# Optimization experiments

Measured on AMD Instinct MI355X. Metric: run time of the kernel, lower is better.

Reference implementation:

```python
import jax, jax.numpy as jnp
import numpy as np

N = 64        # SSM state size
L = 4096      # sequence / kernel length (l_max)
BH = 4096     # batch * channels


def setup_inputs() -> dict:
    key = jax.random.key(0)
    ks = jax.random.split(key, 8)
    u = jax.random.normal(ks[0], (BH, L), dtype=jnp.float32)
    # S4D-Lin style eigenvalue init: Re = -0.5, Im = pi * n
    Lambda_re = -0.5 * jnp.ones((N,), dtype=jnp.float32)
    Lambda_im = jnp.pi * jnp.arange(N, dtype=jnp.float32)
    P_re = jax.random.normal(ks[1], (N,), dtype=jnp.float32) * (0.5 ** 0.5)
    P_im = jax.random.normal(ks[2], (N,), dtype=jnp.float32) * (0.5 ** 0.5)
    B_re = jax.random.normal(ks[3], (N,), dtype=jnp.float32)
    B_im = jax.random.normal(ks[4], (N,), dtype=jnp.float32)
    C_ri = jax.random.normal(ks[5], (N, 2), dtype=jnp.float32) * (0.5 ** 0.5)
    D = jnp.ones((1,), dtype=jnp.float32)
    # log_step ~ uniform(log(0.001), log(0.1)) as in log_step_initializer
    log_step = jax.random.uniform(ks[6], (1,), dtype=jnp.float32,
                                  minval=jnp.log(0.001), maxval=jnp.log(0.1))
    return {"u": u, "Lambda_re": Lambda_re, "Lambda_im": Lambda_im,
            "P_re": P_re, "P_im": P_im, "B_re": B_re, "B_im": B_im,
            "C_ri": C_ri, "D": D, "log_step": log_step}


def kernel_DPLR(Lambda, P, Q, B, C, step, length):
    # Evaluate the SSM generating function at the roots of unity via 4 Cauchy dots,
    # then inverse FFT to recover the length-L convolution kernel.
    Omega_L = jnp.exp((-2j * jnp.pi) * (jnp.arange(length) / length))  # (L,)
    a0, a1 = jnp.conj(C), jnp.conj(Q)
    b0, b1 = B, P
    g = (2.0 / step) * ((1.0 - Omega_L) / (1.0 + Omega_L))  # (L,)
    c = 2.0 / (1.0 + Omega_L)                               # (L,)

    def cauchy(v):  # v: (N,) -> (L,)
        return (v[None, :] / (g[:, None] - Lambda[None, :])).sum(-1)

    k00 = cauchy(a0 * b0)
    k01 = cauchy(a0 * b1)
    k10 = cauchy(a1 * b0)
    k11 = cauchy(a1 * b1)
    at_roots = c * (k00 - k01 * (1.0 / (1.0 + k11)) * k10)
    return jnp.fft.ifft(at_roots, length).real  # (L,)


def causal_convolution(u, K):
    # FFT-based linear (causal) convolution; u: (..., L), K: (L,)
    n = 2 * u.shape[-1]
    ud = jnp.fft.rfft(u, n=n, axis=-1)
    Kd = jnp.fft.rfft(K, n=n)
    return jnp.fft.irfft(ud * Kd, n=n, axis=-1)[..., : u.shape[-1]]


def reference(u, Lambda_re, Lambda_im, P_re, P_im, B_re, B_im, C_ri, D, log_step):
    Lambda = Lambda_re + 1j * Lambda_im
    P = P_re + 1j * P_im
    B = B_re + 1j * B_im
    C = C_ri[..., 0] + 1j * C_ri[..., 1]
    step = jnp.exp(log_step)  # (1,)
    K = kernel_DPLR(Lambda, P, P, B, C, step, u.shape[-1])  # (L,) real
    y_s = causal_convolution(u, K) + D * u  # (BH, L)
    return y_s
```

## Files before the change

### kernel.cpp

```cpp
#include <hip/hip_runtime.h>
#include <math.h>

#define LSEQ 4096
#define MFFT 8192
#define NM   64
#define NBH  4096
#define TMAIN 512

__device__ __forceinline__ float2 cmulf(float2 a, float2 b) {
  return make_float2(a.x*b.x - a.y*b.y, a.x*b.y + a.y*b.x);
}
__device__ __forceinline__ float2 caddf(float2 a, float2 b){ return make_float2(a.x+b.x, a.y+b.y); }
__device__ __forceinline__ float2 csubf(float2 a, float2 b){ return make_float2(a.x-b.x, a.y-b.y); }
__device__ __forceinline__ float2 conjf(float2 a){ return make_float2(a.x, -a.y); }

__device__ __forceinline__ void r4_fwd(float2& x0, float2& x1, float2& x2, float2& x3,
                                       float2 w1, float2 w2, float2 w3) {
  float2 A = caddf(x0,x2), C = csubf(x0,x2);
  float2 B = caddf(x1,x3), D = csubf(x1,x3);
  float2 y1 = make_float2(C.x + D.y, C.y - D.x);
  float2 y3 = make_float2(C.x - D.y, C.y + D.x);
  x0 = caddf(A,B);
  x1 = cmulf(y1,w1);
  x2 = cmulf(csubf(A,B),w2);
  x3 = cmulf(y3,w3);
}
__device__ __forceinline__ void r4_inv(float2& y0, float2& y1, float2& y2, float2& y3,
                                       float2 w1c, float2 w2c, float2 w3c) {
  float2 c1 = cmulf(y1,w1c);
  float2 c2 = cmulf(y2,w2c);
  float2 c3 = cmulf(y3,w3c);
  float2 ap = caddf(y0,c2), bp = csubf(y0,c2);
  float2 cp = caddf(c1,c3);
  float2 dp = make_float2(c3.y - c1.y, c1.x - c3.x);
  y0 = caddf(ap,cp); y1 = caddf(bp,dp); y2 = csubf(ap,cp); y3 = csubf(bp,dp);
}

#define DECL_CONSTS \
  const float C16R[4]={1.f,0.9238795325112867f,0.7071067811865476f,0.3826834323650898f}; \
  const float C16I[4]={0.f,-0.3826834323650898f,-0.7071067811865476f,-0.9238795325112867f}; \
  const float C8R[4] ={1.f,0.7071067811865476f,0.f,-0.7071067811865476f}; \
  const float C8I[4] ={0.f,-0.7071067811865476f,-1.f,-0.7071067811865476f}; \
  const float C163R[4]={1.f,0.3826834323650898f,-0.7071067811865476f,-0.9238795325112867f}; \
  const float C163I[4]={0.f,-0.9238795325112867f,-0.7071067811865476f,0.3826834323650898f};

__device__ __forceinline__ void r16_fwd(float2 x[16], float2 wA) {
  DECL_CONSTS
  float2 wA2 = cmulf(wA,wA), wA3 = cmulf(wA2,wA);
  #pragma unroll
  for (int k0 = 0; k0 < 4; k0++) {
    float2 w1 = cmulf(wA,  make_float2(C16R[k0],C16I[k0]));
    float2 w2 = cmulf(wA2, make_float2(C8R[k0], C8I[k0]));
    float2 w3 = cmulf(wA3, make_float2(C163R[k0],C163I[k0]));
    r4_fwd(x[k0], x[k0+4], x[k0+8], x[k0+12], w1, w2, w3);
  }
  float2 wB = cmulf(wA2,wA2);
  float2 wB2 = cmulf(wB,wB), wB3 = cmulf(wB2,wB);
  #pragma unroll
  for (int q = 0; q < 4; q++)
    r4_fwd(x[4*q], x[4*q+1], x[4*q+2], x[4*q+3], wB, wB2, wB3);
}
__device__ __forceinline__ void r16_inv(float2 x[16], float2 wA) {
  DECL_CONSTS
  float2 wA2 = cmulf(wA,wA), wA3 = cmulf(wA2,wA);
  float2 wB = cmulf(wA2,wA2);
  float2 wB2 = cmulf(wB,wB), wB3 = cmulf(wB2,wB);
  float2 wBc = conjf(wB), wB2c = conjf(wB2), wB3c = conjf(wB3);
  #pragma unroll
  for (int q = 0; q < 4; q++)
    r4_inv(x[4*q], x[4*q+1], x[4*q+2], x[4*q+3], wBc, wB2c, wB3c);
  #pragma unroll
  for (int k0 = 0; k0 < 4; k0++) {
    float2 w1c = conjf(cmulf(wA,  make_float2(C16R[k0],C16I[k0])));
    float2 w2c = conjf(cmulf(wA2, make_float2(C8R[k0], C8I[k0])));
    float2 w3c = conjf(cmulf(wA3, make_float2(C163R[k0],C163I[k0])));
    r4_inv(x[k0], x[k0+4], x[k0+8], x[k0+12], w1c, w2c, w3c);
  }
}

__global__ void tables_kernel(float2* __restrict__ ctg) {
  int t = blockIdx.x*blockDim.x + threadIdx.x;
  if (t >= 560) return;
  int e = (t < 512) ? t : (t < 544) ? 16*(t-512) : 256*(t-544);
  double ang = -2.0*M_PI*(double)e/(double)MFFT;
  ctg[t] = make_float2((float)cos(ang), (float)sin(ang));
}

__global__ void cauchy_kernel(const float* __restrict__ Lre, const float* __restrict__ Lim,
                              const float* __restrict__ Pre, const float* __restrict__ Pim,
                              const float* __restrict__ Bre, const float* __restrict__ Bim,
                              const float* __restrict__ Cri, const float* __restrict__ lstep,
                              float2* __restrict__ a_out) {
  int k = blockIdx.x*blockDim.x + threadIdx.x;
  if (k >= LSEQ) return;
  double step = exp((double)lstep[0]);
  double ang = -2.0*M_PI*(double)k/(double)LSEQ;
  double wr = cos(ang), wi = sin(ang);
  double nr = 1.0 - wr, ni = -wi;
  double dr = 1.0 + wr, di = wi;
  double dn = dr*dr + di*di;
  double gre = (2.0/step) * (nr*dr + ni*di)/dn;
  double gim = (2.0/step) * (ni*dr - nr*di)/dn;
  double cre = 2.0*dr/dn, cim = -2.0*di/dn;
  double k00r=0,k00i=0,k01r=0,k01i=0,k10r=0,k10i=0,k11r=0,k11i=0;
  for (int n = 0; n < NM; n++) {
    double lre = Lre[n], lim = Lim[n];
    double pre = Pre[n], pim = Pim[n];
    double bre = Bre[n], bim = Bim[n];
    double ccr = Cri[2*n], cci = Cri[2*n+1];
    double er = gre - lre, ei = gim - lim;
    double inv = 1.0/(er*er + ei*ei);
    double ir =  er*inv, ii = -ei*inv;
    double v00r = ccr*bre + cci*bim, v00i = ccr*bim - cci*bre;
    double v01r = ccr*pre + cci*pim, v01i = ccr*pim - cci*pre;
    double v10r = pre*bre + pim*bim, v10i = pre*bim - pim*bre;
    double v11r = pre*pre + pim*pim, v11i = 0.0;
    k00r += v00r*ir - v00i*ii;  k00i += v00r*ii + v00i*ir;
    k01r += v01r*ir - v01i*ii;  k01i += v01r*ii + v01i*ir;
    k10r += v10r*ir - v10i*ii;  k10i += v10r*ii + v10i*ir;
    k11r += v11r*ir - v11i*ii;  k11i += v11r*ii + v11i*ir;
  }
  double numr = k01r*k10r - k01i*k10i, numi = k01r*k10i + k01i*k10r;
  double der = 1.0 + k11r, dei = k11i;
  double dinv = 1.0/(der*der + dei*dei);
  double qr = (numr*der + numi*dei)*dinv;
  double qi = (numi*der - numr*dei)*dinv;
  double tr = k00r - qr, ti = k00i - qi;
  double ar = cre*tr - cim*ti, ai = cre*ti + cim*tr;
  a_out[k] = make_float2((float)ar, (float)ai);
}

__global__ void ktime_kernel(const float2* __restrict__ a, float* __restrict__ K) {
  int lane = threadIdx.x & 63;
  int l = blockIdx.x * (blockDim.x >> 6) + (threadIdx.x >> 6);
  if (l >= LSEQ) return;
  double ang0 = 2.0*M_PI*(double)((l*lane) & (LSEQ-1))/(double)LSEQ;
  double tr = cos(ang0), ti = sin(ang0);
  double ang1 = 2.0*M_PI*(double)(l & 63)/64.0;
  double wr = cos(ang1), wi = sin(ang1);
  double acc = 0.0;
  for (int k = 0; k < 64; k++) {
    float2 ak = a[lane + (k << 6)];
    acc += (double)ak.x*tr - (double)ak.y*ti;
    double ntr = tr*wr - ti*wi;
    ti = tr*wi + ti*wr;
    tr = ntr;
  }
  for (int off = 32; off > 0; off >>= 1) acc += __shfl_down(acc, off);
  if (lane == 0) K[l] = (float)(acc/(double)LSEQ);
}

__global__ void kd_kernel(const float* __restrict__ K, const float2* __restrict__ ctg,
                          float2* __restrict__ Kd) {
  __shared__ float2 z[MFFT];
  const int tid = threadIdx.x;
  float2 x[16];
  #pragma unroll
  for (int k = 0; k < 8; k++) x[k] = make_float2(K[tid + 512*k], 0.f);
  #pragma unroll
  for (int k = 8; k < 16; k++) x[k] = make_float2(0.f, 0.f);
  r16_fwd(x, ctg[tid]);
  {
    int xc = (tid >> 5) & 15; int p0 = tid ^ xc;
    #pragma unroll
    for (int k = 0; k < 16; k++) z[p0 + 512*k] = x[k];
  }
  __syncthreads();
  const int j5 = tid & 31;
  const int Gb = (tid >> 5) << 9;
  #pragma unroll
  for (int k = 0; k < 16; k++) x[k] = z[Gb + 32*k + (j5 ^ k)];
  r16_fwd(x, ctg[512 + j5]);
  {
    bool hi = (tid >> 4) & 1;
    float2 w32 = ctg[544 + (tid & 15)];
    float2 weff = hi ? w32 : make_float2(1.f, 0.f);
    float s = hi ? -1.f : 1.f;
    #pragma unroll
    for (int k = 0; k < 16; k++) {
      float rx = __shfl_xor(x[k].x, 16);
      float ry = __shfl_xor(x[k].y, 16);
      float2 pre = make_float2(fmaf(x[k].x, s, rx), fmaf(x[k].y, s, ry));
      x[k] = cmulf(pre, weff);
    }
  }
  #pragma unroll
  for (int k = 0; k < 16; k++) z[Gb + 32*k + (j5 ^ k)] = x[k];
  __syncthreads();
  {
    int xc = (tid >> 1) & 15; int b16 = tid << 4;
    #pragma unroll
    for (int c = 0; c < 16; c++) x[c] = z[b16 + (c ^ xc)];
    r16_fwd(x, make_float2(1.f, 0.f));
    const float sc = 1.0f/(float)MFFT;
    #pragma unroll
    for (int c = 0; c < 16; c++)
      Kd[b16 + c] = make_float2(x[c].x*sc, x[c].y*sc);
  }
}

__global__ __launch_bounds__(TMAIN, 2)
void conv_kernel(const float* __restrict__ u, const float* __restrict__ Dp,
                 const float2* __restrict__ ctg, const float2* __restrict__ Kd,
                 float* __restrict__ out) {
  __shared__ float2 z[MFFT];
  const int tid = threadIdx.x;
  const int r0 = blockIdx.x, r1 = blockIdx.x + (NBH/2);
  const float* u0 = u + (size_t)r0*LSEQ;
  const float* u1 = u + (size_t)r1*LSEQ;
  float2 x[16];
  #pragma unroll
  for (int k = 0; k < 8; k++)
    x[k] = make_float2(u0[tid + 512*k], u1[tid + 512*k]);
  #pragma unroll
  for (int k = 8; k < 16; k++) x[k] = make_float2(0.f, 0.f);
  const float2 wA1 = ctg[tid];
  r16_fwd(x, wA1);
  {
    int xc = (tid >> 5) & 15; int p0 = tid ^ xc;
    #pragma unroll
    for (int k = 0; k < 16; k++) z[p0 + 512*k] = x[k];
  }
  __syncthreads();
  const int j5 = tid & 31;
  const int Gb = (tid >> 5) << 9;
  #pragma unroll
  for (int k = 0; k < 16; k++) x[k] = z[Gb + 32*k + (j5 ^ k)];
  const float2 wA2t = ctg[512 + j5];
  r16_fwd(x, wA2t);
  {
    bool hi = (tid >> 4) & 1;
    float2 w32 = ctg[544 + (tid & 15)];
    float2 weff = hi ? w32 : make_float2(1.f, 0.f);
    float s = hi ? -1.f : 1.f;
    #pragma unroll
    for (int k = 0; k < 16; k++) {
      float rx = __shfl_xor(x[k].x, 16);
      float ry = __shfl_xor(x[k].y, 16);
      float2 pre = make_float2(fmaf(x[k].x, s, rx), fmaf(x[k].y, s, ry));
      x[k] = cmulf(pre, weff);
    }
  }
  #pragma unroll
  for (int k = 0; k < 16; k++) z[Gb + 32*k + (j5 ^ k)] = x[k];
  __syncthreads();
  {
    int xc = (tid >> 1) & 15; int b16 = tid << 4;
    #pragma unroll
    for (int c = 0; c < 16; c++) x[c] = z[b16 + (c ^ xc)];
    float4 kd[8];
    const float4* Kd4 = (const float4*)(Kd + b16);
    #pragma unroll
    for (int q = 0; q < 8; q++) kd[q] = Kd4[q];
    r16_fwd(x, make_float2(1.f, 0.f));
    #pragma unroll
    for (int c = 0; c < 8; c++) {
      x[2*c]   = cmulf(x[2*c],   make_float2(kd[c].x, kd[c].y));
      x[2*c+1] = cmulf(x[2*c+1], make_float2(kd[c].z, kd[c].w));
    }
    r16_inv(x, make_float2(1.f, 0.f));
    #pragma unroll
    for (int c = 0; c < 16; c++) z[b16 + (c ^ xc)] = x[c];
  }
  __syncthreads();
  {
    #pragma unroll
    for (int k = 0; k < 16; k++) x[k] = z[Gb + 32*k + (j5 ^ k)];
    bool hi = (tid >> 4) & 1;
    float2 w32 = ctg[544 + (tid & 15)];
    float2 weffc = hi ? conjf(w32) : make_float2(1.f, 0.f);
    float s = hi ? -1.f : 1.f;
    #pragma unroll
    for (int k = 0; k < 16; k++) {
      float2 v = cmulf(x[k], weffc);
      float rx = __shfl_xor(v.x, 16);
      float ry = __shfl_xor(v.y, 16);
      x[k] = make_float2(fmaf(v.x, s, rx), fmaf(v.y, s, ry));
    }
    r16_inv(x, wA2t);
    #pragma unroll
    for (int k = 0; k < 16; k++) z[Gb + 32*k + (j5 ^ k)] = x[k];
  }
  __syncthreads();
  {
    int xc = (tid >> 5) & 15; int p0 = tid ^ xc;
    #pragma unroll
    for (int k = 0; k < 16; k++) x[k] = z[p0 + 512*k];
    r16_inv(x, wA1);
    const float Dv = Dp[0];
    float* o0 = out + (size_t)r0*LSEQ;
    float* o1 = out + (size_t)r1*LSEQ;
    #pragma unroll
    for (int k = 0; k < 8; k++) {
      int idx = tid + 512*k;
      o0[idx] = x[k].x + Dv*u0[idx];
      o1[idx] = x[k].y + Dv*u1[idx];
    }
  }
}

extern "C" void kernel_launch(void* const* d_in, const int* in_sizes, int n_in,
                              void* d_out, int out_size, void* d_ws, size_t ws_size,
                              hipStream_t stream) {
  const float* u     = (const float*)d_in[0];
  const float* Lre   = (const float*)d_in[1];
  const float* Lim   = (const float*)d_in[2];
  const float* Pre   = (const float*)d_in[3];
  const float* Pim   = (const float*)d_in[4];
  const float* Bre   = (const float*)d_in[5];
  const float* Bim   = (const float*)d_in[6];
  const float* Cri   = (const float*)d_in[7];
  const float* Dp    = (const float*)d_in[8];
  const float* lstep = (const float*)d_in[9];
  float* out = (float*)d_out;

  char* ws = (char*)d_ws;
  float2* a_ws  = (float2*)(ws);
  float*  K_ws  = (float*)(ws + 32768);
  float2* Kd_ws = (float2*)(ws + 49152);
  float2* ct_ws = (float2*)(ws + 114688);

  hipLaunchKernelGGL(tables_kernel, dim3(3),    dim3(256), 0, stream, ct_ws);
  hipLaunchKernelGGL(cauchy_kernel, dim3(64),   dim3(64),  0, stream,
                     Lre, Lim, Pre, Pim, Bre, Bim, Cri, lstep, a_ws);
  hipLaunchKernelGGL(ktime_kernel,  dim3(1024), dim3(256), 0, stream, a_ws, K_ws);
  hipLaunchKernelGGL(kd_kernel,     dim3(1),    dim3(TMAIN), 0, stream,
                     K_ws, ct_ws, Kd_ws);
  hipLaunchKernelGGL(conv_kernel,   dim3(NBH/2), dim3(TMAIN), 0, stream,
                     u, Dp, ct_ws, Kd_ws, out);
}
```

Measured before the change: 126.2 us.

## Fold D skip into kernel spectrum, precompute twiddle tables, use wave barriers

```diff
diff --git a/kernel.cpp b/kernel.cpp
--- a/kernel.cpp
+++ b/kernel.cpp
@@ -9,6 +9,9 @@
 
 __device__ __forceinline__ float2 cmulf(float2 a, float2 b) {
   return make_float2(a.x*b.x - a.y*b.y, a.x*b.y + a.y*b.x);
+}
+__device__ __forceinline__ float2 cmulc(float2 a, float2 b) {
+  return make_float2(a.x*b.x + a.y*b.y, a.y*b.x - a.x*b.y);
 }
 __device__ __forceinline__ float2 caddf(float2 a, float2 b){ return make_float2(a.x+b.x, a.y+b.y); }
 __device__ __forceinline__ float2 csubf(float2 a, float2 b){ return make_float2(a.x-b.x, a.y-b.y); }
@@ -35,6 +38,16 @@
   float2 dp = make_float2(c3.y - c1.y, c1.x - c3.x);
   y0 = caddf(ap,cp); y1 = caddf(bp,dp); y2 = csubf(ap,cp); y3 = csubf(bp,dp);
 }
+__device__ __forceinline__ void r4_invc(float2& y0, float2& y1, float2& y2, float2& y3,
+                                        float2 w1, float2 w2, float2 w3) {
+  float2 c1 = cmulc(y1,w1);
+  float2 c2 = cmulc(y2,w2);
+  float2 c3 = cmulc(y3,w3);
+  float2 ap = caddf(y0,c2), bp = csubf(y0,c2);
+  float2 cp = caddf(c1,c3);
+  float2 dp = make_float2(c3.y - c1.y, c1.x - c3.x);
+  y0 = caddf(ap,cp); y1 = caddf(bp,dp); y2 = csubf(ap,cp); y3 = csubf(bp,dp);
+}
 
 #define DECL_CONSTS \
   const float C16R[4]={1.f,0.9238795325112867f,0.7071067811865476f,0.3826834323650898f}; \
@@ -44,46 +57,97 @@
   const float C163R[4]={1.f,0.3826834323650898f,-0.7071067811865476f,-0.9238795325112867f}; \
   const float C163I[4]={0.f,-0.9238795325112867f,-0.7071067811865476f,0.3826834323650898f};
 
-__device__ __forceinline__ void r16_fwd(float2 x[16], float2 wA) {
+__device__ __forceinline__ void r16_fwd1(float2 x[16]) {
   DECL_CONSTS
-  float2 wA2 = cmulf(wA,wA), wA3 = cmulf(wA2,wA);
-  #pragma unroll
-  for (int k0 = 0; k0 < 4; k0++) {
-    float2 w1 = cmulf(wA,  make_float2(C16R[k0],C16I[k0]));
-    float2 w2 = cmulf(wA2, make_float2(C8R[k0], C8I[k0]));
-    float2 w3 = cmulf(wA3, make_float2(C163R[k0],C163I[k0]));
-    r4_fwd(x[k0], x[k0+4], x[k0+8], x[k0+12], w1, w2, w3);
-  }
-  float2 wB = cmulf(wA2,wA2);
-  float2 wB2 = cmulf(wB,wB), wB3 = cmulf(wB2,wB);
+  #pragma unroll
+  for (int k0 = 0; k0 < 4; k0++)
+    r4_fwd(x[k0], x[k0+4], x[k0+8], x[k0+12],
+           make_float2(C16R[k0],C16I[k0]), make_float2(C8R[k0],C8I[k0]),
+           make_float2(C163R[k0],C163I[k0]));
   #pragma unroll
   for (int q = 0; q < 4; q++)
-    r4_fwd(x[4*q], x[4*q+1], x[4*q+2], x[4*q+3], wB, wB2, wB3);
-}
-__device__ __forceinline__ void r16_inv(float2 x[16], float2 wA) {
+    r4_fwd(x[4*q], x[4*q+1], x[4*q+2], x[4*q+3],
+           make_float2(1.f,0.f), make_float2(1.f,0.f), make_float2(1.f,0.f));
+}
+__device__ __forceinline__ void r16_inv1(float2 x[16]) {
   DECL_CONSTS
-  float2 wA2 = cmulf(wA,wA), wA3 = cmulf(wA2,wA);
-  float2 wB = cmulf(wA2,wA2);
-  float2 wB2 = cmulf(wB,wB), wB3 = cmulf(wB2,wB);
-  float2 wBc = conjf(wB), wB2c = conjf(wB2), wB3c = conjf(wB3);
   #pragma unroll
   for (int q = 0; q < 4; q++)
-    r4_inv(x[4*q], x[4*q+1], x[4*q+2], x[4*q+3], wBc, wB2c, wB3c);
-  #pragma unroll
-  for (int k0 = 0; k0 < 4; k0++) {
-    float2 w1c = conjf(cmulf(wA,  make_float2(C16R[k0],C16I[k0])));
-    float2 w2c = conjf(cmulf(wA2, make_float2(C8R[k0], C8I[k0])));
-    float2 w3c = conjf(cmulf(wA3, make_float2(C163R[k0],C163I[k0])));
-    r4_inv(x[k0], x[k0+4], x[k0+8], x[k0+12], w1c, w2c, w3c);
-  }
-}
-
-__global__ void tables_kernel(float2* __restrict__ ctg) {
+    r4_invc(x[4*q], x[4*q+1], x[4*q+2], x[4*q+3],
+            make_float2(1.f,0.f), make_float2(1.f,0.f), make_float2(1.f,0.f));
+  #pragma unroll
+  for (int k0 = 0; k0 < 4; k0++)
+    r4_invc(x[k0], x[k0+4], x[k0+8], x[k0+12],
+            make_float2(C16R[k0],C16I[k0]), make_float2(C8R[k0],C8I[k0]),
+            make_float2(C163R[k0],C163I[k0]));
+}
+
+__device__ __forceinline__ void r16_fwd_t(float2 x[16], const float4 tp[8]) {
+  float2 tw[16];
+  #pragma unroll
+  for (int q = 0; q < 8; q++) {
+    tw[2*q]   = make_float2(tp[q].x, tp[q].y);
+    tw[2*q+1] = make_float2(tp[q].z, tp[q].w);
+  }
+  #pragma unroll
+  for (int k0 = 0; k0 < 4; k0++)
+    r4_fwd(x[k0], x[k0+4], x[k0+8], x[k0+12], tw[k0], tw[4+k0], tw[8+k0]);
+  #pragma unroll
+  for (int q = 0; q < 4; q++)
+    r4_fwd(x[4*q], x[4*q+1], x[4*q+2], x[4*q+3], tw[12], tw[13], tw[14]);
+}
+__device__ __forceinline__ void r16_inv_t(float2 x[16], const float4 tp[8]) {
+  float2 tw[16];
+  #pragma unroll
+  for (int q = 0; q < 8; q++) {
+    tw[2*q]   = make_float2(tp[q].x, tp[q].y);
+    tw[2*q+1] = make_float2(tp[q].z, tp[q].w);
+  }
+  #pragma unroll
+  for (int q = 0; q < 4; q++)
+    r4_invc(x[4*q], x[4*q+1], x[4*q+2], x[4*q+3], tw[12], tw[13], tw[14]);
+  #pragma unroll
+  for (int k0 = 0; k0 < 4; k0++)
+    r4_invc(x[k0], x[k0+4], x[k0+8], x[k0+12], tw[k0], tw[4+k0], tw[8+k0]);
+}
+
+__device__ __forceinline__ float2 Wexp(long long e) {
+  double ang = -2.0*M_PI*(double)(e & (MFFT-1))/(double)MFFT;
+  return make_float2((float)cos(ang), (float)sin(ang));
+}
+__global__ void tables_kernel(float4* __restrict__ tp1, float4* __restrict__ tp2,
+                              float2* __restrict__ ct2) {
   int t = blockIdx.x*blockDim.x + threadIdx.x;
-  if (t >= 560) return;
-  int e = (t < 512) ? t : (t < 544) ? 16*(t-512) : 256*(t-544);
-  double ang = -2.0*M_PI*(double)e/(double)MFFT;
-  ctg[t] = make_float2((float)cos(ang), (float)sin(ang));
+  if (t < 512) {
+    float2 w[16];
+    #pragma unroll
+    for (int i = 0; i < 4; i++) {
+      w[i]   = Wexp((long long)t   + 512LL*i);
+      w[4+i] = Wexp(2LL*t + 1024LL*i);
+      w[8+i] = Wexp(3LL*t + 1536LL*i);
+    }
+    w[12] = Wexp(4LL*t); w[13] = Wexp(8LL*t); w[14] = Wexp(12LL*t);
+    w[15] = make_float2(1.f, 0.f);
+    #pragma unroll
+    for (int q = 0; q < 8; q++)
+      tp1[q*512 + t] = make_float4(w[2*q].x, w[2*q].y, w[2*q+1].x, w[2*q+1].y);
+  } else if (t < 544) {
+    int j = t - 512;
+    float2 w[16];
+    #pragma unroll
+    for (int i = 0; i < 4; i++) {
+      w[i]   = Wexp(16LL*j + 512LL*i);
+      w[4+i] = Wexp(32LL*j + 1024LL*i);
+      w[8+i] = Wexp(48LL*j + 1536LL*i);
+    }
+    w[12] = Wexp(64LL*j); w[13] = Wexp(128LL*j); w[14] = Wexp(192LL*j);
+    w[15] = make_float2(1.f, 0.f);
+    #pragma unroll
+    for (int q = 0; q < 8; q++)
+      tp2[q*32 + j] = make_float4(w[2*q].x, w[2*q].y, w[2*q+1].x, w[2*q+1].y);
+  } else if (t < 560) {
+    ct2[t - 544] = Wexp(256LL*(t - 544));
+  }
 }
 
 __global__ void cauchy_kernel(const float* __restrict__ Lre, const float* __restrict__ Lim,
@@ -150,16 +214,24 @@
   if (lane == 0) K[l] = (float)(acc/(double)LSEQ);
 }
 
-__global__ void kd_kernel(const float* __restrict__ K, const float2* __restrict__ ctg,
-                          float2* __restrict__ Kd) {
+__global__ void kd_kernel(const float* __restrict__ K, const float* __restrict__ Dp,
+                          const float4* __restrict__ tp1, const float4* __restrict__ tp2,
+                          const float2* __restrict__ ct2, float2* __restrict__ Kd) {
   __shared__ float2 z[MFFT];
   const int tid = threadIdx.x;
   float2 x[16];
-  #pragma unroll
-  for (int k = 0; k < 8; k++) x[k] = make_float2(K[tid + 512*k], 0.f);
+  float4 tpr[8];
+  #pragma unroll
+  for (int q = 0; q < 8; q++) tpr[q] = tp1[(q<<9) + tid];
+  #pragma unroll
+  for (int k = 0; k < 8; k++) {
+    float v = K[tid + 512*k];
+    if (tid == 0 && k == 0) v += Dp[0];
+    x[k] = make_float2(v, 0.f);
+  }
   #pragma unroll
   for (int k = 8; k < 16; k++) x[k] = make_float2(0.f, 0.f);
-  r16_fwd(x, ctg[tid]);
+  r16_fwd_t(x, tpr);
   {
     int xc = (tid >> 5) & 15; int p0 = tid ^ xc;
     #pragma unroll
@@ -168,12 +240,15 @@
   __syncthreads();
   const int j5 = tid & 31;
   const int Gb = (tid >> 5) << 9;
+  float4 tq[8];
+  #pragma unroll
+  for (int q = 0; q < 8; q++) tq[q] = tp2[(q<<5) + j5];
   #pragma unroll
   for (int k = 0; k < 16; k++) x[k] = z[Gb + 32*k + (j5 ^ k)];
-  r16_fwd(x, ctg[512 + j5]);
+  r16_fwd_t(x, tq);
   {
     bool hi = (tid >> 4) & 1;
-    float2 w32 = ctg[544 + (tid & 15)];
+    float2 w32 = ct2[tid & 15];
     float2 weff = hi ? w32 : make_float2(1.f, 0.f);
     float s = hi ? -1.f : 1.f;
     #pragma unroll
@@ -191,7 +266,7 @@
     int xc = (tid >> 1) & 15; int b16 = tid << 4;
     #pragma unroll
     for (int c = 0; c < 16; c++) x[c] = z[b16 + (c ^ xc)];
-    r16_fwd(x, make_float2(1.f, 0.f));
+    r16_fwd1(x);
     const float sc = 1.0f/(float)MFFT;
     #pragma unroll
     for (int c = 0; c < 16; c++)
@@ -200,8 +275,9 @@
 }
 
 __global__ __launch_bounds__(TMAIN, 2)
-void conv_kernel(const float* __restrict__ u, const float* __restrict__ Dp,
-                 const float2* __restrict__ ctg, const float2* __restrict__ Kd,
+void conv_kernel(const float* __restrict__ u,
+                 const float4* __restrict__ tp1, const float4* __restrict__ tp2,
+                 const float2* __restrict__ ct2, const float2* __restrict__ Kd,
                  float* __restrict__ out) {
   __shared__ float2 z[MFFT];
   const int tid = threadIdx.x;
@@ -209,14 +285,16 @@
   const float* u0 = u + (size_t)r0*LSEQ;
   const float* u1 = u + (size_t)r1*LSEQ;
   float2 x[16];
-  #pragma unroll
-  for (int k = 0; k < 8; k++)
-    x[k] = make_float2(u0[tid + 512*k], u1[tid + 512*k]);
-  #pragma unroll
-  for (int k = 8; k < 16; k++) x[k] = make_float2(0.f, 0.f);
-  const float2 wA1 = ctg[tid];
-  r16_fwd(x, wA1);
-  {
+  {
+    float4 tpr[8];
+    #pragma unroll
+    for (int q = 0; q < 8; q++) tpr[q] = tp1[(q<<9) + tid];
+    #pragma unroll
+    for (int k = 0; k < 8; k++)
+      x[k] = make_float2(u0[tid + 512*k], u1[tid + 512*k]);
+    #pragma unroll
+    for (int k = 8; k < 16; k++) x[k] = make_float2(0.f, 0.f);
+    r16_fwd_t(x, tpr);
     int xc = (tid >> 5) & 15; int p0 = tid ^ xc;
     #pragma unroll
     for (int k = 0; k < 16; k++) z[p0 + 512*k] = x[k];
@@ -224,26 +302,28 @@
   __syncthreads();
   const int j5 = tid & 31;
   const int Gb = (tid >> 5) << 9;
-  #pragma unroll
-  for (int k = 0; k < 16; k++) x[k] = z[Gb + 32*k + (j5 ^ k)];
-  const float2 wA2t = ctg[512 + j5];
-  r16_fwd(x, wA2t);
-  {
-    bool hi = (tid >> 4) & 1;
-    float2 w32 = ctg[544 + (tid & 15)];
+  const bool hi = (tid >> 4) & 1;
+  const float2 w32 = ct2[tid & 15];
+  const float sgn = hi ? -1.f : 1.f;
+  {
+    float4 tq[8];
+    #pragma unroll
+    for (int q = 0; q < 8; q++) tq[q] = tp2[(q<<5) + j5];
+    #pragma unroll
+    for (int k = 0; k < 16; k++) x[k] = z[Gb + 32*k + (j5 ^ k)];
+    r16_fwd_t(x, tq);
     float2 weff = hi ? w32 : make_float2(1.f, 0.f);
-    float s = hi ? -1.f : 1.f;
     #pragma unroll
     for (int k = 0; k < 16; k++) {
       float rx = __shfl_xor(x[k].x, 16);
       float ry = __shfl_xor(x[k].y, 16);
-      float2 pre = make_float2(fmaf(x[k].x, s, rx), fmaf(x[k].y, s, ry));
+      float2 pre = make_float2(fmaf(x[k].x, sgn, rx), fmaf(x[k].y, sgn, ry));
       x[k] = cmulf(pre, weff);
     }
-  }
-  #pragma unroll
-  for (int k = 0; k < 16; k++) z[Gb + 32*k + (j5 ^ k)] = x[k];
-  __syncthreads();
+    #pragma unroll
+    for (int k = 0; k < 16; k++) z[Gb + 32*k + (j5 ^ k)] = x[k];
+  }
+  __builtin_amdgcn_wave_barrier();
   {
     int xc = (tid >> 1) & 15; int b16 = tid << 4;
     #pragma unroll
@@ -252,49 +332,51 @@
     const float4* Kd4 = (const float4*)(Kd + b16);
     #pragma unroll
     for (int q = 0; q < 8; q++) kd[q] = Kd4[q];
-    r16_fwd(x, make_float2(1.f, 0.f));
+    r16_fwd1(x);
     #pragma unroll
     for (int c = 0; c < 8; c++) {
       x[2*c]   = cmulf(x[2*c],   make_float2(kd[c].x, kd[c].y));
       x[2*c+1] = cmulf(x[2*c+1], make_float2(kd[c].z, kd[c].w));
     }
-    r16_inv(x, make_float2(1.f, 0.f));
+    r16_inv1(x);
     #pragma unroll
     for (int c = 0; c < 16; c++) z[b16 + (c ^ xc)] = x[c];
   }
-  __syncthreads();
+  __builtin_amdgcn_wave_barrier();
   {
     #pragma unroll
     for (int k = 0; k < 16; k++) x[k] = z[Gb + 32*k + (j5 ^ k)];
-    bool hi = (tid >> 4) & 1;
-    float2 w32 = ctg[544 + (tid & 15)];
     float2 weffc = hi ? conjf(w32) : make_float2(1.f, 0.f);
-    float s = hi ? -1.f : 1.f;
     #pragma unroll
     for (int k = 0; k < 16; k++) {
       float2 v = cmulf(x[k], weffc);
       float rx = __shfl_xor(v.x, 16);
       float ry = __shfl_xor(v.y, 16);
-      x[k] = make_float2(fmaf(v.x, s, rx), fmaf(v.y, s, ry));
-    }
-    r16_inv(x, wA2t);
+      x[k] = make_float2(fmaf(v.x, sgn, rx), fmaf(v.y, sgn, ry));
+    }
+    float4 tq[8];
+    #pragma unroll
+    for (int q = 0; q < 8; q++) tq[q] = tp2[(q<<5) + j5];
+    r16_inv_t(x, tq);
     #pragma unroll
     for (int k = 0; k < 16; k++) z[Gb + 32*k + (j5 ^ k)] = x[k];
   }
   __syncthreads();
   {
+    float4 tpr[8];
+    #pragma unroll
+    for (int q = 0; q < 8; q++) tpr[q] = tp1[(q<<9) + tid];
     int xc = (tid >> 5) & 15; int p0 = tid ^ xc;
     #pragma unroll
     for (int k = 0; k < 16; k++) x[k] = z[p0 + 512*k];
-    r16_inv(x, wA1);
-    const float Dv = Dp[0];
+    r16_inv_t(x, tpr);
     float* o0 = out + (size_t)r0*LSEQ;
     float* o1 = out + (size_t)r1*LSEQ;
     #pragma unroll
     for (int k = 0; k < 8; k++) {
       int idx = tid + 512*k;
-      o0[idx] = x[k].x + Dv*u0[idx];
-      o1[idx] = x[k].y + Dv*u1[idx];
+      o0[idx] = x[k].x;
+      o1[idx] = x[k].y;
     }
   }
 }
@@ -318,14 +400,17 @@
   float2* a_ws  = (float2*)(ws);
   float*  K_ws  = (float*)(ws + 32768);
   float2* Kd_ws = (float2*)(ws + 49152);
-  float2* ct_ws = (float2*)(ws + 114688);
-
-  hipLaunchKernelGGL(tables_kernel, dim3(3),    dim3(256), 0, stream, ct_ws);
+  float4* tp1_ws= (float4*)(ws + 114688);
+  float4* tp2_ws= (float4*)(ws + 180224);
+  float2* ct2_ws= (float2*)(ws + 184320);
+
+  hipLaunchKernelGGL(tables_kernel, dim3(3),    dim3(256), 0, stream,
+                     tp1_ws, tp2_ws, ct2_ws);
   hipLaunchKernelGGL(cauchy_kernel, dim3(64),   dim3(64),  0, stream,
                      Lre, Lim, Pre, Pim, Bre, Bim, Cri, lstep, a_ws);
   hipLaunchKernelGGL(ktime_kernel,  dim3(1024), dim3(256), 0, stream, a_ws, K_ws);
   hipLaunchKernelGGL(kd_kernel,     dim3(1),    dim3(TMAIN), 0, stream,
-                     K_ws, ct_ws, Kd_ws);
+                     K_ws, Dp, tp1_ws, tp2_ws, ct2_ws, Kd_ws);
   hipLaunchKernelGGL(conv_kernel,   dim3(NBH/2), dim3(TMAIN), 0, stream,
-                     u, Dp, ct_ws, Kd_ws, out);
-}
+                     u, tp1_ws, tp2_ws, ct2_ws, Kd_ws, out);
+}
```

New measurement: 131.0 us. 3.9% more time.

## Restructure FFT convolution as radix-8 with 1024 threads and precomputed twiddle tables

Applied to the files above, without the earlier changes.

```diff
diff --git a/kernel.cpp b/kernel.cpp
--- a/kernel.cpp
+++ b/kernel.cpp
@@ -5,85 +5,115 @@
 #define MFFT 8192
 #define NM   64
 #define NBH  4096
-#define TMAIN 512
 
 __device__ __forceinline__ float2 cmulf(float2 a, float2 b) {
   return make_float2(a.x*b.x - a.y*b.y, a.x*b.y + a.y*b.x);
 }
+__device__ __forceinline__ float2 cmulc(float2 a, float2 b) {
+  return make_float2(a.x*b.x + a.y*b.y, a.y*b.x - a.x*b.y);
+}
 __device__ __forceinline__ float2 caddf(float2 a, float2 b){ return make_float2(a.x+b.x, a.y+b.y); }
 __device__ __forceinline__ float2 csubf(float2 a, float2 b){ return make_float2(a.x-b.x, a.y-b.y); }
-__device__ __forceinline__ float2 conjf(float2 a){ return make_float2(a.x, -a.y); }
-
-__device__ __forceinline__ void r4_fwd(float2& x0, float2& x1, float2& x2, float2& x3,
-                                       float2 w1, float2 w2, float2 w3) {
-  float2 A = caddf(x0,x2), C = csubf(x0,x2);
-  float2 B = caddf(x1,x3), D = csubf(x1,x3);
-  float2 y1 = make_float2(C.x + D.y, C.y - D.x);
-  float2 y3 = make_float2(C.x - D.y, C.y + D.x);
-  x0 = caddf(A,B);
-  x1 = cmulf(y1,w1);
-  x2 = cmulf(csubf(A,B),w2);
-  x3 = cmulf(y3,w3);
-}
-__device__ __forceinline__ void r4_inv(float2& y0, float2& y1, float2& y2, float2& y3,
-                                       float2 w1c, float2 w2c, float2 w3c) {
-  float2 c1 = cmulf(y1,w1c);
-  float2 c2 = cmulf(y2,w2c);
-  float2 c3 = cmulf(y3,w3c);
-  float2 ap = caddf(y0,c2), bp = csubf(y0,c2);
-  float2 cp = caddf(c1,c3);
-  float2 dp = make_float2(c3.y - c1.y, c1.x - c3.x);
-  y0 = caddf(ap,cp); y1 = caddf(bp,dp); y2 = csubf(ap,cp); y3 = csubf(bp,dp);
-}
-
-#define DECL_CONSTS \
-  const float C16R[4]={1.f,0.9238795325112867f,0.7071067811865476f,0.3826834323650898f}; \
-  const float C16I[4]={0.f,-0.3826834323650898f,-0.7071067811865476f,-0.9238795325112867f}; \
-  const float C8R[4] ={1.f,0.7071067811865476f,0.f,-0.7071067811865476f}; \
-  const float C8I[4] ={0.f,-0.7071067811865476f,-1.f,-0.7071067811865476f}; \
-  const float C163R[4]={1.f,0.3826834323650898f,-0.7071067811865476f,-0.9238795325112867f}; \
-  const float C163I[4]={0.f,-0.9238795325112867f,-0.7071067811865476f,0.3826834323650898f};
-
-__device__ __forceinline__ void r16_fwd(float2 x[16], float2 wA) {
-  DECL_CONSTS
-  float2 wA2 = cmulf(wA,wA), wA3 = cmulf(wA2,wA);
-  #pragma unroll
-  for (int k0 = 0; k0 < 4; k0++) {
-    float2 w1 = cmulf(wA,  make_float2(C16R[k0],C16I[k0]));
-    float2 w2 = cmulf(wA2, make_float2(C8R[k0], C8I[k0]));
-    float2 w3 = cmulf(wA3, make_float2(C163R[k0],C163I[k0]));
-    r4_fwd(x[k0], x[k0+4], x[k0+8], x[k0+12], w1, w2, w3);
-  }
-  float2 wB = cmulf(wA2,wA2);
-  float2 wB2 = cmulf(wB,wB), wB3 = cmulf(wB2,wB);
-  #pragma unroll
-  for (int q = 0; q < 4; q++)
-    r4_fwd(x[4*q], x[4*q+1], x[4*q+2], x[4*q+3], wB, wB2, wB3);
-}
-__device__ __forceinline__ void r16_inv(float2 x[16], float2 wA) {
-  DECL_CONSTS
-  float2 wA2 = cmulf(wA,wA), wA3 = cmulf(wA2,wA);
-  float2 wB = cmulf(wA2,wA2);
-  float2 wB2 = cmulf(wB,wB), wB3 = cmulf(wB2,wB);
-  float2 wBc = conjf(wB), wB2c = conjf(wB2), wB3c = conjf(wB3);
-  #pragma unroll
-  for (int q = 0; q < 4; q++)
-    r4_inv(x[4*q], x[4*q+1], x[4*q+2], x[4*q+3], wBc, wB2c, wB3c);
-  #pragma unroll
-  for (int k0 = 0; k0 < 4; k0++) {
-    float2 w1c = conjf(cmulf(wA,  make_float2(C16R[k0],C16I[k0])));
-    float2 w2c = conjf(cmulf(wA2, make_float2(C8R[k0], C8I[k0])));
-    float2 w3c = conjf(cmulf(wA3, make_float2(C163R[k0],C163I[k0])));
-    r4_inv(x[k0], x[k0+4], x[k0+8], x[k0+12], w1c, w2c, w3c);
-  }
-}
-
-__global__ void tables_kernel(float2* __restrict__ ctg) {
-  int t = blockIdx.x*blockDim.x + threadIdx.x;
-  if (t >= 560) return;
-  int e = (t < 512) ? t : (t < 544) ? 16*(t-512) : 256*(t-544);
-  double ang = -2.0*M_PI*(double)e/(double)MFFT;
-  ctg[t] = make_float2((float)cos(ang), (float)sin(ang));
+
+__device__ __forceinline__ int ZS(int i){ return i ^ ((i>>4)&15) ^ (((i>>8)&15)<<4); }
+
+__device__ __forceinline__ void dft8_fwd(float2 x[8]) {
+  const float RC = 0.7071067811865476f;
+  float2 u0=caddf(x[0],x[4]), v0=csubf(x[0],x[4]);
+  float2 u1=caddf(x[1],x[5]), d1=csubf(x[1],x[5]);
+  float2 u2=caddf(x[2],x[6]), d2=csubf(x[2],x[6]);
+  float2 u3=caddf(x[3],x[7]), d3=csubf(x[3],x[7]);
+  float2 v1 = make_float2(RC*(d1.x + d1.y), RC*(d1.y - d1.x));
+  float2 v2 = make_float2(d2.y, -d2.x);
+  float2 v3 = make_float2(RC*(d3.y - d3.x), -RC*(d3.x + d3.y));
+  float2 p0=caddf(u0,u2), q0=csubf(u0,u2);
+  float2 p1=caddf(u1,u3), qt=csubf(u1,u3);
+  float2 q1 = make_float2(qt.y, -qt.x);
+  float2 r0=caddf(v0,v2), s0=csubf(v0,v2);
+  float2 r1=caddf(v1,v3), st=csubf(v1,v3);
+  float2 s1 = make_float2(st.y, -st.x);
+  x[0]=caddf(p0,p1); x[4]=csubf(p0,p1);
+  x[2]=caddf(q0,q1); x[6]=csubf(q0,q1);
+  x[1]=caddf(r0,r1); x[5]=csubf(r0,r1);
+  x[3]=caddf(s0,s1); x[7]=csubf(s0,s1);
+}
+__device__ __forceinline__ void dft8_inv(float2 x[8]) {
+  const float RC = 0.7071067811865476f;
+  float2 p0=caddf(x[0],x[4]), p1=csubf(x[0],x[4]);
+  float2 q0=caddf(x[2],x[6]), q1=csubf(x[2],x[6]);
+  float2 r0=caddf(x[1],x[5]), r1=csubf(x[1],x[5]);
+  float2 s0=caddf(x[3],x[7]), s1=csubf(x[3],x[7]);
+  float2 q1i = make_float2(-q1.y, q1.x);
+  float2 s1i = make_float2(-s1.y, s1.x);
+  float2 u0=caddf(p0,q0), u2=csubf(p0,q0);
+  float2 u1=caddf(p1,q1i), u3=csubf(p1,q1i);
+  float2 v0=caddf(r0,s0), v2=csubf(r0,s0);
+  float2 v1=caddf(r1,s1i), v3=csubf(r1,s1i);
+  float2 w1 = make_float2(RC*(v1.x - v1.y), RC*(v1.x + v1.y));
+  float2 w2 = make_float2(-v2.y, v2.x);
+  float2 w3 = make_float2(-RC*(v3.x + v3.y), RC*(v3.x - v3.y));
+  x[0]=caddf(u0,v0); x[4]=csubf(u0,v0);
+  x[1]=caddf(u1,w1); x[5]=csubf(u1,w1);
+  x[2]=caddf(u2,w2); x[6]=csubf(u2,w2);
+  x[3]=caddf(u3,w3); x[7]=csubf(u3,w3);
+}
+
+__device__ __forceinline__ void tw_fwd(float2 x[8], const float4* __restrict__ T, int J, int j) {
+  float4 a0 = T[j],       a1 = T[J+j];
+  x[1]=cmulf(x[1],make_float2(a0.x,a0.y));
+  x[2]=cmulf(x[2],make_float2(a0.z,a0.w));
+  x[3]=cmulf(x[3],make_float2(a1.x,a1.y));
+  x[4]=cmulf(x[4],make_float2(a1.z,a1.w));
+  float4 a2 = T[2*J+j],   a3 = T[3*J+j];
+  x[5]=cmulf(x[5],make_float2(a2.x,a2.y));
+  x[6]=cmulf(x[6],make_float2(a2.z,a2.w));
+  x[7]=cmulf(x[7],make_float2(a3.x,a3.y));
+}
+__device__ __forceinline__ void tw_inv(float2 x[8], const float4* __restrict__ T, int J, int j) {
+  float4 a0 = T[j],       a1 = T[J+j];
+  x[1]=cmulc(x[1],make_float2(a0.x,a0.y));
+  x[2]=cmulc(x[2],make_float2(a0.z,a0.w));
+  x[3]=cmulc(x[3],make_float2(a1.x,a1.y));
+  x[4]=cmulc(x[4],make_float2(a1.z,a1.w));
+  float4 a2 = T[2*J+j],   a3 = T[3*J+j];
+  x[5]=cmulc(x[5],make_float2(a2.x,a2.y));
+  x[6]=cmulc(x[6],make_float2(a2.z,a2.w));
+  x[7]=cmulc(x[7],make_float2(a3.x,a3.y));
+}
+
+#define DECL_W16C \
+  const float2 W16C[8] = { make_float2(1.f,0.f), \
+    make_float2(0.9238795325112867f,-0.3826834323650898f), \
+    make_float2(0.7071067811865476f,-0.7071067811865476f), \
+    make_float2(0.3826834323650898f,-0.9238795325112867f), \
+    make_float2(0.f,-1.f), \
+    make_float2(-0.3826834323650898f,-0.9238795325112867f), \
+    make_float2(-0.7071067811865476f,-0.7071067811865476f), \
+    make_float2(-0.9238795325112867f,-0.3826834323650898f) };
+
+__device__ __forceinline__ float2 W8192e(long long e) {
+  double ang = -2.0*M_PI*(double)(e & (MFFT-1))/(double)MFFT;
+  return make_float2((float)cos(ang), (float)sin(ang));
+}
+__global__ void tables8_kernel(float4* __restrict__ T1, float4* __restrict__ T2,
+                               float4* __restrict__ T3) {
+  int idx = blockIdx.x*blockDim.x + threadIdx.x;
+  if (idx < 4096) {
+    int q = idx >> 10, j = idx & 1023;
+    float2 wa = W8192e((long long)j*(2*q+1));
+    float2 wb = W8192e((long long)j*(2*q+2));
+    T1[(q<<10)+j] = make_float4(wa.x, wa.y, wb.x, wb.y);
+  } else if (idx < 4608) {
+    int r = idx - 4096; int q = r >> 7, j = r & 127;
+    float2 wa = W8192e(8LL*j*(2*q+1));
+    float2 wb = W8192e(8LL*j*(2*q+2));
+    T2[(q<<7)+j] = make_float4(wa.x, wa.y, wb.x, wb.y);
+  } else if (idx < 4672) {
+    int r = idx - 4608; int q = r >> 4, j = r & 15;
+    float2 wa = W8192e(64LL*j*(2*q+1));
+    float2 wb = W8192e(64LL*j*(2*q+2));
+    T3[(q<<4)+j] = make_float4(wa.x, wa.y, wb.x, wb.y);
+  }
 }
 
 __global__ void cauchy_kernel(const float* __restrict__ Lre, const float* __restrict__ Lim,
@@ -150,151 +180,199 @@
   if (lane == 0) K[l] = (float)(acc/(double)LSEQ);
 }
 
-__global__ void kd_kernel(const float* __restrict__ K, const float2* __restrict__ ctg,
-                          float2* __restrict__ Kd) {
+__global__ void kd8_kernel(const float* __restrict__ K, const float* __restrict__ Dp,
+                           const float4* __restrict__ T1, const float4* __restrict__ T2,
+                           const float4* __restrict__ T3,
+                           float2* __restrict__ KdE, float2* __restrict__ KdO) {
   __shared__ float2 z[MFFT];
-  const int tid = threadIdx.x;
-  float2 x[16];
+  const int t = threadIdx.x;
+  float2 x[8];
   #pragma unroll
-  for (int k = 0; k < 8; k++) x[k] = make_float2(K[tid + 512*k], 0.f);
+  for (int k = 0; k < 4; k++) {
+    float v = K[t + (k<<10)];
+    if (t == 0 && k == 0) v += Dp[0];
+    x[k] = make_float2(v, 0.f);
+  }
   #pragma unroll
-  for (int k = 8; k < 16; k++) x[k] = make_float2(0.f, 0.f);
-  r16_fwd(x, ctg[tid]);
-  {
-    int xc = (tid >> 5) & 15; int p0 = tid ^ xc;
-    #pragma unroll
-    for (int k = 0; k < 16; k++) z[p0 + 512*k] = x[k];
-  }
-  __syncthreads();
-  const int j5 = tid & 31;
-  const int Gb = (tid >> 5) << 9;
+  for (int k = 4; k < 8; k++) x[k] = make_float2(0.f, 0.f);
+  dft8_fwd(x); tw_fwd(x, T1, 1024, t);
   #pragma unroll
-  for (int k = 0; k < 16; k++) x[k] = z[Gb + 32*k + (j5 ^ k)];
-  r16_fwd(x, ctg[512 + j5]);
-  {
-    bool hi = (tid >> 4) & 1;
-    float2 w32 = ctg[544 + (tid & 15)];
-    float2 weff = hi ? w32 : make_float2(1.f, 0.f);
-    float s = hi ? -1.f : 1.f;
-    #pragma unroll
-    for (int k = 0; k < 16; k++) {
-      float rx = __shfl_xor(x[k].x, 16);
-      float ry = __shfl_xor(x[k].y, 16);
-      float2 pre = make_float2(fmaf(x[k].x, s, rx), fmaf(x[k].y, s, ry));
-      x[k] = cmulf(pre, weff);
-    }
-  }
-  #pragma unroll
-  for (int k = 0; k < 16; k++) z[Gb + 32*k + (j5 ^ k)] = x[k];
-  __syncthreads();
-  {
-    int xc = (tid >> 1) & 15; int b16 = tid << 4;
-    #pragma unroll
-    for (int c = 0; c < 16; c++) x[c] = z[b16 + (c ^ xc)];
-    r16_fwd(x, make_float2(1.f, 0.f));
-    const float sc = 1.0f/(float)MFFT;
-    #pragma unroll
-    for (int c = 0; c < 16; c++)
-      Kd[b16 + c] = make_float2(x[c].x*sc, x[c].y*sc);
-  }
-}
-
-__global__ __launch_bounds__(TMAIN, 2)
-void conv_kernel(const float* __restrict__ u, const float* __restrict__ Dp,
-                 const float2* __restrict__ ctg, const float2* __restrict__ Kd,
-                 float* __restrict__ out) {
+  for (int m = 0; m < 8; m++) z[ZS(t + (m<<10))] = x[m];
+  __syncthreads();
+  {
+    const int j2 = t & 127, gb2 = (t>>7)<<10;
+    int ai[8];
+    #pragma unroll
+    for (int m = 0; m < 8; m++) ai[m] = ZS(gb2 + j2 + (m<<7));
+    #pragma unroll
+    for (int m = 0; m < 8; m++) x[m] = z[ai[m]];
+    dft8_fwd(x); tw_fwd(x, T2, 128, j2);
+    #pragma unroll
+    for (int m = 0; m < 8; m++) z[ai[m]] = x[m];
+  }
+  __syncthreads();
+  {
+    const int j3 = t & 15, gb3 = (t>>4)<<7;
+    int ai[8];
+    #pragma unroll
+    for (int m = 0; m < 8; m++) ai[m] = ZS(gb3 + j3 + (m<<4));
+    #pragma unroll
+    for (int m = 0; m < 8; m++) x[m] = z[ai[m]];
+    dft8_fwd(x); tw_fwd(x, T3, 16, j3);
+    #pragma unroll
+    for (int m = 0; m < 8; m++) z[ai[m]] = x[m];
+  }
+  __builtin_amdgcn_wave_barrier();
+  {
+    DECL_W16C
+    const int G4 = t>>1, j1 = t & 1, gb4 = G4<<4;
+    #pragma unroll
+    for (int m = 0; m < 8; m++) x[m] = z[ZS(gb4 + j1 + (m<<1))];
+    dft8_fwd(x);
+    #pragma unroll
+    for (int m = 1; m < 8; m++) {
+      float2 wm = j1 ? W16C[m] : make_float2(1.f, 0.f);
+      x[m] = cmulf(x[m], wm);
+    }
+    const float sc = 1.0f/8192.0f;
+    float2* kout = (j1 ? KdO : KdE) + (G4<<3);
+    #pragma unroll
+    for (int p = 0; p < 8; p++) {
+      float ox = __shfl_xor(x[p].x, 1);
+      float oy = __shfl_xor(x[p].y, 1);
+      float2 v = j1 ? make_float2(ox - x[p].x, oy - x[p].y)
+                    : make_float2(x[p].x + ox, x[p].y + oy);
+      kout[p] = make_float2(v.x*sc, v.y*sc);
+    }
+  }
+}
+
+__global__ __launch_bounds__(1024, 4)
+void conv8_kernel(const float* __restrict__ u,
+                  const float4* __restrict__ T1, const float4* __restrict__ T2,
+                  const float4* __restrict__ T3,
+                  const float2* __restrict__ KdE, const float2* __restrict__ KdO,
+                  float* __restrict__ out) {
   __shared__ float2 z[MFFT];
-  const int tid = threadIdx.x;
+  const int t = threadIdx.x;
   const int r0 = blockIdx.x, r1 = blockIdx.x + (NBH/2);
   const float* u0 = u + (size_t)r0*LSEQ;
   const float* u1 = u + (size_t)r1*LSEQ;
-  float2 x[16];
-  #pragma unroll
-  for (int k = 0; k < 8; k++)
-    x[k] = make_float2(u0[tid + 512*k], u1[tid + 512*k]);
-  #pragma unroll
-  for (int k = 8; k < 16; k++) x[k] = make_float2(0.f, 0.f);
-  const float2 wA1 = ctg[tid];
-  r16_fwd(x, wA1);
-  {
-    int xc = (tid >> 5) & 15; int p0 = tid ^ xc;
-    #pragma unroll
-    for (int k = 0; k < 16; k++) z[p0 + 512*k] = x[k];
-  }
-  __syncthreads();
-  const int j5 = tid & 31;
-  const int Gb = (tid >> 5) << 9;
-  #pragma unroll
-  for (int k = 0; k < 16; k++) x[k] = z[Gb + 32*k + (j5 ^ k)];
-  const float2 wA2t = ctg[512 + j5];
-  r16_fwd(x, wA2t);
-  {
-    bool hi = (tid >> 4) & 1;
-    float2 w32 = ctg[544 + (tid & 15)];
-    float2 weff = hi ? w32 : make_float2(1.f, 0.f);
-    float s = hi ? -1.f : 1.f;
-    #pragma unroll
-    for (int k = 0; k < 16; k++) {
-      float rx = __shfl_xor(x[k].x, 16);
-      float ry = __shfl_xor(x[k].y, 16);
-      float2 pre = make_float2(fmaf(x[k].x, s, rx), fmaf(x[k].y, s, ry));
-      x[k] = cmulf(pre, weff);
-    }
-  }
-  #pragma unroll
-  for (int k = 0; k < 16; k++) z[Gb + 32*k + (j5 ^ k)] = x[k];
-  __syncthreads();
-  {
-    int xc = (tid >> 1) & 15; int b16 = tid << 4;
-    #pragma unroll
-    for (int c = 0; c < 16; c++) x[c] = z[b16 + (c ^ xc)];
-    float4 kd[8];
-    const float4* Kd4 = (const float4*)(Kd + b16);
-    #pragma unroll
-    for (int q = 0; q < 8; q++) kd[q] = Kd4[q];
-    r16_fwd(x, make_float2(1.f, 0.f));
-    #pragma unroll
-    for (int c = 0; c < 8; c++) {
-      x[2*c]   = cmulf(x[2*c],   make_float2(kd[c].x, kd[c].y));
-      x[2*c+1] = cmulf(x[2*c+1], make_float2(kd[c].z, kd[c].w));
-    }
-    r16_inv(x, make_float2(1.f, 0.f));
-    #pragma unroll
-    for (int c = 0; c < 16; c++) z[b16 + (c ^ xc)] = x[c];
-  }
-  __syncthreads();
-  {
-    #pragma unroll
-    for (int k = 0; k < 16; k++) x[k] = z[Gb + 32*k + (j5 ^ k)];
-    bool hi = (tid >> 4) & 1;
-    float2 w32 = ctg[544 + (tid & 15)];
-    float2 weffc = hi ? conjf(w32) : make_float2(1.f, 0.f);
-    float s = hi ? -1.f : 1.f;
-    #pragma unroll
-    for (int k = 0; k < 16; k++) {
-      float2 v = cmulf(x[k], weffc);
-      float rx = __shfl_xor(v.x, 16);
-      float ry = __shfl_xor(v.y, 16);
-      x[k] = make_float2(fmaf(v.x, s, rx), fmaf(v.y, s, ry));
-    }
-    r16_inv(x, wA2t);
-    #pragma unroll
-    for (int k = 0; k < 16; k++) z[Gb + 32*k + (j5 ^ k)] = x[k];
-  }
-  __syncthreads();
-  {
-    int xc = (tid >> 5) & 15; int p0 = tid ^ xc;
-    #pragma unroll
-    for (int k = 0; k < 16; k++) x[k] = z[p0 + 512*k];
-    r16_inv(x, wA1);
-    const float Dv = Dp[0];
+  float2 x[8];
+  {
+    #pragma unroll
+    for (int k = 0; k < 4; k++)
+      x[k] = make_float2(u0[t + (k<<10)], u1[t + (k<<10)]);
+    #pragma unroll
+    for (int k = 4; k < 8; k++) x[k] = make_float2(0.f, 0.f);
+    dft8_fwd(x); tw_fwd(x, T1, 1024, t);
+    #pragma unroll
+    for (int m = 0; m < 8; m++) z[ZS(t + (m<<10))] = x[m];
+  }
+  __syncthreads();
+  const int j2 = t & 127, gb2 = (t>>7)<<10;
+  {
+    int ai[8];
+    #pragma unroll
+    for (int m = 0; m < 8; m++) ai[m] = ZS(gb2 + j2 + (m<<7));
+    #pragma unroll
+    for (int m = 0; m < 8; m++) x[m] = z[ai[m]];
+    dft8_fwd(x); tw_fwd(x, T2, 128, j2);
+    #pragma unroll
+    for (int m = 0; m < 8; m++) z[ai[m]] = x[m];
+  }
+  __syncthreads();
+  const int j3 = t & 15, gb3 = (t>>4)<<7;
+  {
+    int ai[8];
+    #pragma unroll
+    for (int m = 0; m < 8; m++) ai[m] = ZS(gb3 + j3 + (m<<4));
+    #pragma unroll
+    for (int m = 0; m < 8; m++) x[m] = z[ai[m]];
+    dft8_fwd(x); tw_fwd(x, T3, 16, j3);
+    #pragma unroll
+    for (int m = 0; m < 8; m++) z[ai[m]] = x[m];
+  }
+  __builtin_amdgcn_wave_barrier();
+  {
+    DECL_W16C
+    const int G4 = t>>1, j1 = t & 1, gb4 = G4<<4;
+    int ai[8];
+    #pragma unroll
+    for (int m = 0; m < 8; m++) ai[m] = ZS(gb4 + j1 + (m<<1));
+    #pragma unroll
+    for (int m = 0; m < 8; m++) x[m] = z[ai[m]];
+    dft8_fwd(x);
+    #pragma unroll
+    for (int m = 1; m < 8; m++) {
+      float2 wm = j1 ? W16C[m] : make_float2(1.f, 0.f);
+      x[m] = cmulf(x[m], wm);
+    }
+    const float4* kp = (const float4*)((j1 ? KdO : KdE) + (G4<<3));
+    #pragma unroll
+    for (int p2 = 0; p2 < 4; p2++) {
+      float4 kq = kp[p2];
+      #pragma unroll
+      for (int s = 0; s < 2; s++) {
+        const int p = 2*p2 + s;
+        float2 kd = s ? make_float2(kq.z, kq.w) : make_float2(kq.x, kq.y);
+        float ox = __shfl_xor(x[p].x, 1);
+        float oy = __shfl_xor(x[p].y, 1);
+        float2 v = j1 ? make_float2(ox - x[p].x, oy - x[p].y)
+                      : make_float2(x[p].x + ox, x[p].y + oy);
+        x[p] = cmulf(v, kd);
+      }
+    }
+    #pragma unroll
+    for (int p = 0; p < 8; p++) {
+      float ox = __shfl_xor(x[p].x, 1);
+      float oy = __shfl_xor(x[p].y, 1);
+      x[p] = j1 ? make_float2(ox - x[p].x, oy - x[p].y)
+                : make_float2(x[p].x + ox, x[p].y + oy);
+    }
+    #pragma unroll
+    for (int m = 1; m < 8; m++) {
+      float2 wm = j1 ? W16C[m] : make_float2(1.f, 0.f);
+      x[m] = cmulc(x[m], wm);
+    }
+    dft8_inv(x);
+    #pragma unroll
+    for (int m = 0; m < 8; m++) z[ai[m]] = x[m];
+  }
+  __builtin_amdgcn_wave_barrier();
+  {
+    int ai[8];
+    #pragma unroll
+    for (int m = 0; m < 8; m++) ai[m] = ZS(gb3 + j3 + (m<<4));
+    #pragma unroll
+    for (int m = 0; m < 8; m++) x[m] = z[ai[m]];
+    tw_inv(x, T3, 16, j3); dft8_inv(x);
+    #pragma unroll
+    for (int m = 0; m < 8; m++) z[ai[m]] = x[m];
+  }
+  __syncthreads();
+  {
+    int ai[8];
+    #pragma unroll
+    for (int m = 0; m < 8; m++) ai[m] = ZS(gb2 + j2 + (m<<7));
+    #pragma unroll
+    for (int m = 0; m < 8; m++) x[m] = z[ai[m]];
+    tw_inv(x, T2, 128, j2); dft8_inv(x);
+    #pragma unroll
+    for (int m = 0; m < 8; m++) z[ai[m]] = x[m];
+  }
+  __syncthreads();
+  {
+    #pragma unroll
+    for (int m = 0; m < 8; m++) x[m] = z[ZS(t + (m<<10))];
+    tw_inv(x, T1, 1024, t); dft8_inv(x);
     float* o0 = out + (size_t)r0*LSEQ;
     float* o1 = out + (size_t)r1*LSEQ;
     #pragma unroll
-    for (int k = 0; k < 8; k++) {
-      int idx = tid + 512*k;
-      o0[idx] = x[k].x + Dv*u0[idx];
-      o1[idx] = x[k].y + Dv*u1[idx];
+    for (int m = 0; m < 4; m++) {
+      int idx = t + (m<<10);
+      o0[idx] = x[m].x;
+      o1[idx] = x[m].y;
     }
   }
 }
@@ -315,17 +393,21 @@
   float* out = (float*)d_out;
 
   char* ws = (char*)d_ws;
-  float2* a_ws  = (float2*)(ws);
-  float*  K_ws  = (float*)(ws + 32768);
-  float2* Kd_ws = (float2*)(ws + 49152);
-  float2* ct_ws = (float2*)(ws + 114688);
-
-  hipLaunchKernelGGL(tables_kernel, dim3(3),    dim3(256), 0, stream, ct_ws);
-  hipLaunchKernelGGL(cauchy_kernel, dim3(64),   dim3(64),  0, stream,
+  float2* a_ws   = (float2*)(ws);
+  float*  K_ws   = (float*)(ws + 32768);
+  float2* KdE_ws = (float2*)(ws + 49152);
+  float2* KdO_ws = (float2*)(ws + 81920);
+  float4* T1_ws  = (float4*)(ws + 114688);
+  float4* T2_ws  = (float4*)(ws + 180224);
+  float4* T3_ws  = (float4*)(ws + 188416);
+
+  hipLaunchKernelGGL(tables8_kernel, dim3(19),   dim3(256), 0, stream,
+                     T1_ws, T2_ws, T3_ws);
+  hipLaunchKernelGGL(cauchy_kernel,  dim3(64),   dim3(64),  0, stream,
                      Lre, Lim, Pre, Pim, Bre, Bim, Cri, lstep, a_ws);
-  hipLaunchKernelGGL(ktime_kernel,  dim3(1024), dim3(256), 0, stream, a_ws, K_ws);
-  hipLaunchKernelGGL(kd_kernel,     dim3(1),    dim3(TMAIN), 0, stream,
-                     K_ws, ct_ws, Kd_ws);
-  hipLaunchKernelGGL(conv_kernel,   dim3(NBH/2), dim3(TMAIN), 0, stream,
-                     u, Dp, ct_ws, Kd_ws, out);
-}
+  hipLaunchKernelGGL(ktime_kernel,   dim3(1024), dim3(256), 0, stream, a_ws, K_ws);
+  hipLaunchKernelGGL(kd8_kernel,     dim3(1),    dim3(1024), 0, stream,
+                     K_ws, Dp, T1_ws, T2_ws, T3_ws, KdE_ws, KdO_ws);
+  hipLaunchKernelGGL(conv8_kernel,   dim3(NBH/2), dim3(1024), 0, stream,
+                     u, T1_ws, T2_ws, T3_ws, KdE_ws, KdO_ws, out);
+}
```

Measured after the change: 118.3 us. 1.07x faster.
